# Optimization experiments

Measured on AMD Instinct MI355X. Metric: run time of the kernel, lower is better.

The kernel has to match this reference:

```python
import jax, jax.numpy as jnp
import numpy as np

K = 20

def lrelu(x):
    return jnp.where(x >= 0, x, 0.2 * x)

def get_graph_feature(x, k):
    # x: (B, N, C) channel-last. Returns (B, N, k, 2C) = [neighbor - x, x].
    inner = jnp.einsum('bnc,bmc->bnm', x, x)          # (B, N, N)
    sq = jnp.sum(x * x, axis=-1)                       # (B, N)
    # negative squared distance; top-k gives nearest neighbors (incl. self)
    neg_dist = 2.0 * inner - sq[:, :, None] - sq[:, None, :]
    _, idx = jax.lax.top_k(neg_dist, k)                # (B, N, k)
    neigh = jnp.take_along_axis(x[:, None, :, :], idx[:, :, :, None], axis=2)  # (B, N, k, C)
    center = jnp.broadcast_to(x[:, :, None, :], neigh.shape)
    return jnp.concatenate([neigh - center, center], axis=-1)

def setup_inputs() -> dict:
    key = jax.random.key(0)
    ks = jax.random.split(key, 12)
    B, N, input_dim = 32, 2048, 6
    emb_dim, out_dim = 1024, 40
    def w(k_, shape):
        fan_in = shape[-1]
        return jax.random.normal(k_, shape, dtype=jnp.float32) * (1.0 / np.sqrt(fan_in))
    return {
        'x':  jax.random.normal(ks[0], (B, N, input_dim), dtype=jnp.float32),
        'W1': w(ks[1], (64, 6)),            # conv1: 1x1 conv, no bias
        'W2': w(ks[2], (64, 128)),          # conv2
        'W5': w(ks[3], (emb_dim, 128)),     # conv5 (1d)
        'W3': w(ks[4], (32, input_dim - 3)),# conv3
        'W4': w(ks[5], (64, 32)),           # conv4
        'L1': w(ks[6], (128, (emb_dim + 64) * 2)),  # linear1, no bias
        'L2w': w(ks[7], (64, 128)),
        'L2b': jnp.zeros((64,), dtype=jnp.float32),
        'L3w': w(ks[8], (out_dim, 64)),
        'L3b': jnp.zeros((out_dim,), dtype=jnp.float32),
    }

def reference(x, W1, W2, W5, W3, W4, L1, L2w, L2b, L3w, L3b):
    x_pos = x[:, :, :3]       # (B, N, 3)
    x_feat = x[:, :, 3:]      # (B, N, input_dim-3)

    # EdgeConv block 1
    e = get_graph_feature(x_pos, K)                       # (B, N, k, 6)
    e = lrelu(jnp.einsum('bnkc,oc->bnko', e, W1))         # (B, N, k, 64)
    x1 = jnp.max(e, axis=2)                               # (B, N, 64)

    # EdgeConv block 2
    e = get_graph_feature(x1, K)                          # (B, N, k, 128)
    e = lrelu(jnp.einsum('bnkc,oc->bnko', e, W2))         # (B, N, k, 64)
    x2 = jnp.max(e, axis=2)                               # (B, N, 64)

    # conv5 over concatenated features
    h = jnp.concatenate([x1, x2], axis=-1)                # (B, N, 128)
    h = lrelu(jnp.einsum('bnc,oc->bno', h, W5))           # (B, N, emb)
    g = jnp.concatenate([jnp.max(h, axis=1), jnp.mean(h, axis=1)], axis=-1)  # (B, 2*emb)

    # per-point feature MLP (conv3 -> conv4)
    f = lrelu(jnp.einsum('bnc,oc->bno', x_feat, W3))      # (B, N, 32)
    f = lrelu(jnp.einsum('bnc,oc->bno', f, W4))           # (B, N, 64)
    fg = jnp.concatenate([jnp.max(f, axis=1), jnp.mean(f, axis=1)], axis=-1)  # (B, 128)

    z = jnp.concatenate([g, fg], axis=-1)                 # (B, (emb+64)*2)
    z = lrelu(z @ L1.T)
    z = lrelu(z @ L2w.T + L2b)
    return z @ L3w.T + L3b                                # (B, output)
```

## Files before the change

### kernel.cpp

```cpp
#include <hip/hip_runtime.h>
#include <math.h>

#define B_ 32
#define N_ 2048
#define KNN 20
#define FINF 3.402823466e38f
#define SCAP 192

typedef __attribute__((ext_vector_type(8))) short short8;
typedef __attribute__((ext_vector_type(4))) float f32x4;

#define OFF_X1   ((size_t)0)
#define OFF_X2   (OFF_X1 + (size_t)B_*N_*64*4)
#define OFF_SQ1  (OFF_X2 + (size_t)B_*N_*64*4)
#define OFF_IDX1 (OFF_SQ1 + (size_t)B_*N_*4)
#define OFF_IDX2 (OFF_IDX1 + (size_t)B_*N_*KNN*4)
#define OFF_PMAX (OFF_IDX2 + (size_t)B_*N_*KNN*4)
#define OFF_PSUM (OFF_PMAX + (size_t)B_*16*1024*4)
#define OFF_G    (OFF_PSUM + (size_t)B_*16*1024*4)
#define OFF_FG   (OFF_G + (size_t)B_*2048*4)
#define OFF_DIST (OFF_FG + (size_t)B_*128*4)
#define OFF_P    OFF_DIST
#define OFF_Q    (OFF_P   + (size_t)B_*N_*64*4)
#define OFF_XHI  (OFF_Q   + (size_t)B_*N_*64*4)
#define OFF_XLO  (OFF_XHI + (size_t)B_*N_*128*2)
#define OFF_WHI  OFF_IDX1
#define OFF_WLO  (OFF_WHI + (size_t)1024*128*2)

__device__ __forceinline__ float lrelu(float x) { return x >= 0.0f ? x : 0.2f * x; }

__device__ __forceinline__ void bf16split(float a, unsigned short& hi, unsigned short& lo) {
    unsigned u = __float_as_uint(a);
    unsigned r16 = (u + 0x7fffu + ((u >> 16) & 1u)) >> 16;
    hi = (unsigned short)r16;
    float l = a - __uint_as_float(r16 << 16);
    unsigned ul = __float_as_uint(l);
    lo = (unsigned short)((ul + 0x7fffu + ((ul >> 16) & 1u)) >> 16);
}

template<class F>
__device__ __forceinline__ void wave_top20_slow(const float (&v)[32], int lane, int* out20, F idxf) {
    unsigned alive = 0xffffffffu;
    for (int sel = 0; sel < 20; ++sel) {
        float bv = -FINF;
        int bm = 0x7fffffff;
#pragma unroll
        for (int j = 0; j < 32; ++j) {
            bool a = (alive >> j) & 1u;
            bool better = a && (v[j] > bv);
            bv = better ? v[j] : bv;
            bm = better ? idxf(j) : bm;
        }
#pragma unroll
        for (int off = 32; off; off >>= 1) {
            float ov = __shfl_xor(bv, off, 64);
            int   om = __shfl_xor(bm, off, 64);
            bool take = (ov > bv) || (ov == bv && om < bm);
            bv = take ? ov : bv;
            bm = take ? om : bm;
        }
        if (lane == 0) out20[sel] = bm;
#pragma unroll
        for (int j = 0; j < 32; ++j)
            if (idxf(j) == bm) alive &= ~(1u << j);
    }
}

template<class F>
__device__ __forceinline__ void wave_top20_fast(const float (&v)[32], int lane,
                                                float* sval, int* sidx, int* out20, F idxf) {
    float lm = v[0];
#pragma unroll
    for (int j = 1; j < 32; ++j) lm = fmaxf(lm, v[j]);
    float s = lm;
#pragma unroll
    for (int k = 2; k <= 64; k <<= 1) {
#pragma unroll
        for (int j2 = k >> 1; j2 > 0; j2 >>= 1) {
            float o = __shfl_xor(s, j2, 64);
            bool up = ((lane & k) == 0);
            bool high = ((lane & j2) != 0);
            s = (high == up) ? fmaxf(s, o) : fminf(s, o);
        }
    }
    float that = __shfl(s, 44, 64);
    int cnt = 0;
    unsigned long long below = (lane == 63) ? 0xffffffffffffffffull >> 1
                                            : ((1ull << lane) - 1ull);
#pragma unroll
    for (int j = 0; j < 32; ++j) {
        bool p = (v[j] >= that);
        unsigned long long mk = __ballot(p);
        if (p) {
            int slot = cnt + (int)__popcll(mk & below);
            if (slot < SCAP) { sval[slot] = v[j]; sidx[slot] = idxf(j); }
        }
        cnt += (int)__popcll(mk);
    }
    int S = cnt;
    if (S > SCAP) {
        wave_top20_slow(v, lane, out20, idxf);
        return;
    }
    if (S <= 64) {
        bool ok = lane < S;
        float cv = ok ? sval[lane] : -FINF;
        int   cm = ok ? sidx[lane] : 0x7fffffff;
#pragma unroll
        for (int k = 2; k <= 64; k <<= 1) {
#pragma unroll
            for (int j2 = k >> 1; j2 > 0; j2 >>= 1) {
                float ov = __shfl_xor(cv, j2, 64);
                int   om = __shfl_xor(cm, j2, 64);
                bool up = ((lane & k) == 0);
                bool high = ((lane & j2) != 0);
                bool cur_first = (cv > ov) || (cv == ov && cm < om);
                bool take = (high == up) ? cur_first : !cur_first;
                cv = take ? ov : cv;
                cm = take ? om : cm;
            }
        }
        if (lane < 20) out20[lane] = cm;
    } else {
        float cv[3]; int cm[3]; unsigned alive = 0;
#pragma unroll
        for (int r = 0; r < 3; ++r) {
            int i = r * 64 + lane;
            bool ok = i < S;
            float vv = sval[i];
            int   mm = sidx[i];
            cv[r] = ok ? vv : -FINF;
            cm[r] = ok ? mm : 0x7fffffff;
            if (ok) alive |= 1u << r;
        }
        for (int sel = 0; sel < 20; ++sel) {
            float bv = -FINF; int bm = 0x7fffffff;
#pragma unroll
            for (int r = 0; r < 3; ++r) {
                bool a = (alive >> r) & 1u;
                bool better = a && (cv[r] > bv || (cv[r] == bv && cm[r] < bm));
                bv = better ? cv[r] : bv;
                bm = better ? cm[r] : bm;
            }
#pragma unroll
            for (int off = 32; off; off >>= 1) {
                float ov = __shfl_xor(bv, off, 64);
                int   om = __shfl_xor(bm, off, 64);
                bool take = (ov > bv) || (ov == bv && om < bm);
                bv = take ? ov : bv;
                bm = take ? om : bm;
            }
            if (lane == 0) out20[sel] = bm;
#pragma unroll
            for (int r = 0; r < 3; ++r)
                if (cm[r] == bm) alive &= ~(1u << r);
        }
    }
}

__global__ __launch_bounds__(256) void k12_knn_conv1(const float* __restrict__ x,
                                                     const float* __restrict__ W1,
                                                     float* __restrict__ x1,
                                                     float* __restrict__ sq1) {
    __shared__ float sP[N_ * 3];
    __shared__ float sval[4][SCAP];
    __shared__ int   sidx[4][SCAP];
    __shared__ int   sOut[4][20];
    int tid = threadIdx.x;
    int wid = tid >> 6, lane = tid & 63;
    int row = blockIdx.x * 4 + wid;
    int b = row >> 11, n = row & 2047;
    const float* xb = x + (size_t)b * N_ * 6;
    for (int m = tid; m < N_; m += 256) {
        float4 f = *(const float4*)(xb + m * 6);
        sP[m*3+0] = f.x; sP[m*3+1] = f.y; sP[m*3+2] = f.z;
    }
    __syncthreads();
    float cx = sP[n*3+0], cy = sP[n*3+1], cz = sP[n*3+2];
    float sqn = cx*cx + cy*cy + cz*cz;
    float v[32];
#pragma unroll
    for (int j = 0; j < 32; ++j) {
        int m = lane + (j << 6);
        float mx_ = sP[m*3+0], my = sP[m*3+1], mz = sP[m*3+2];
        float inner = cx*mx_ + cy*my + cz*mz;
        float sqm = mx_*mx_ + my*my + mz*mz;
        v[j] = 2.0f*inner - sqn - sqm;
    }
    wave_top20_fast(v, lane, sval[wid], sidx[wid], sOut[wid],
                    [lane](int j) { return lane + (j << 6); });
    int o = lane;
    float w0 = W1[o*6+0], w1 = W1[o*6+1], w2 = W1[o*6+2];
    float w3 = W1[o*6+3], w4 = W1[o*6+4], w5 = W1[o*6+5];
    float base = w3*cx + w4*cy + w5*cz;
    float mx = -FINF;
#pragma unroll
    for (int k = 0; k < KNN; ++k) {
        int m = sOut[wid][k];
        float dx = sP[m*3+0]-cx, dy = sP[m*3+1]-cy, dz = sP[m*3+2]-cz;
        float s = base + w0*dx + w1*dy + w2*dz;
        mx = fmaxf(mx, lrelu(s));
    }
    x1[(size_t)row*64 + o] = mx;
    float sq = mx*mx;
#pragma unroll
    for (int off = 32; off; off >>= 1) sq += __shfl_xor(sq, off, 64);
    if (o == 0) sq1[row] = sq;
}

__global__ __launch_bounds__(256) void k3_dist(const float* __restrict__ x1,
                                               const float* __restrict__ sq1,
                                               float* __restrict__ dist, int b0) {
    __shared__ float sA[32][128];
    __shared__ float sB[32][128];
    int t = blockIdx.x;
    int I = (int)((sqrtf(8.0f*t + 1.0f) - 1.0f) * 0.5f);
    while ((I+1)*(I+2)/2 <= t) ++I;
    while (I*(I+1)/2 > t) --I;
    int J = t - I*(I+1)/2;
    int b = b0 + blockIdx.y;
    const float* Xb  = x1  + (size_t)b * N_ * 64;
    const float* sqb = sq1 + (size_t)b * N_;
    float* Db = dist + (size_t)blockIdx.y * N_ * N_;
    int i0 = I*128, j0 = J*128;
    int tid = threadIdx.x;
    float acc[8][8] = {};
    for (int kt = 0; kt < 64; kt += 32) {
#pragma unroll
        for (int l = 0; l < 4; ++l) {
            int v = l*256 + tid;
            int i = v >> 3, cg = (v & 7) << 2;
            float4 fa = *(const float4*)(Xb + (size_t)(i0+i)*64 + kt + cg);
            sA[cg+0][i] = fa.x; sA[cg+1][i] = fa.y; sA[cg+2][i] = fa.z; sA[cg+3][i] = fa.w;
            float4 fb = *(const float4*)(Xb + (size_t)(j0+i)*64 + kt + cg);
            sB[cg+0][i] = fb.x; sB[cg+1][i] = fb.y; sB[cg+2][i] = fb.z; sB[cg+3][i] = fb.w;
        }
        __syncthreads();
        int ti = (tid & 15) * 8, tj = (tid >> 4) * 8;
#pragma unroll 4
        for (int c = 0; c < 32; ++c) {
            float a[8], w[8];
            *(float4*)&a[0] = *(const float4*)&sA[c][ti];
            *(float4*)&a[4] = *(const float4*)&sA[c][ti+4];
            *(float4*)&w[0] = *(const float4*)&sB[c][tj];
            *(float4*)&w[4] = *(const float4*)&sB[c][tj+4];
#pragma unroll
            for (int ii = 0; ii < 8; ++ii)
#pragma unroll
                for (int jj = 0; jj < 8; ++jj)
                    acc[ii][jj] = fmaf(a[ii], w[jj], acc[ii][jj]);
        }
        __syncthreads();
    }
    int ti = (tid & 15) * 8, tj = (tid >> 4) * 8;
    float sqi[8], sqj[8];
#pragma unroll
    for (int ii = 0; ii < 8; ++ii) sqi[ii] = sqb[i0 + ti + ii];
#pragma unroll
    for (int jj = 0; jj < 8; ++jj) sqj[jj] = sqb[j0 + tj + jj];
#pragma unroll
    for (int ii = 0; ii < 8; ++ii) {
        float ov[8];
#pragma unroll
        for (int jj = 0; jj < 8; ++jj) ov[jj] = 2.0f*acc[ii][jj] - sqi[ii] - sqj[jj];
        float4* p = (float4*)(Db + (size_t)(i0+ti+ii)*N_ + j0 + tj);
        p[0] = *(float4*)&ov[0]; p[1] = *(float4*)&ov[4];
    }
    if (I != J) {
#pragma unroll
        for (int jj = 0; jj < 8; ++jj) {
            float ov[8];
#pragma unroll
            for (int ii = 0; ii < 8; ++ii) ov[ii] = 2.0f*acc[ii][jj] - sqi[ii] - sqj[jj];
            float4* p = (float4*)(Db + (size_t)(j0+tj+jj)*N_ + i0 + ti);
            p[0] = *(float4*)&ov[0]; p[1] = *(float4*)&ov[4];
        }
    }
}

__global__ __launch_bounds__(256) void k4_topk(const float* __restrict__ dist,
                                               int* __restrict__ idx2, int b0) {
    __shared__ float sval[4][SCAP];
    __shared__ int   sidx[4][SCAP];
    __shared__ int   sOut[4][20];
    int wid = threadIdx.x >> 6, lane = threadIdx.x & 63;
    int lrow = blockIdx.x * 4 + wid;
    int lb = lrow >> 11, n = lrow & 2047;
    const float4* Dr4 = (const float4*)(dist + (size_t)lb * N_ * N_ + (size_t)n * N_);
    float v[32];
#pragma unroll
    for (int j4 = 0; j4 < 8; ++j4) {
        float4 f = Dr4[(j4 << 6) + lane];
        v[j4*4+0] = f.x; v[j4*4+1] = f.y; v[j4*4+2] = f.z; v[j4*4+3] = f.w;
    }
    wave_top20_fast(v, lane, sval[wid], sidx[wid], sOut[wid],
                    [lane](int j) { return (lane << 2) + ((j >> 2) << 8) + (j & 3); });
    int row = (b0 + lb) * N_ + n;
    if (lane < 20) idx2[(size_t)row*KNN + lane] = sOut[wid][lane];
}

__global__ __launch_bounds__(256) void k5pre_pq(const float* __restrict__ x1,
                                                const float* __restrict__ W2,
                                                float* __restrict__ P,
                                                float* __restrict__ Q,
                                                const float* __restrict__ W5,
                                                unsigned short* __restrict__ Whi,
                                                unsigned short* __restrict__ Wlo) {
    if (blockIdx.x >= 512) {
        int e = (blockIdx.x - 512) * 256 + threadIdx.x;
        int r = e >> 5, c4 = (e & 31) << 2;
        float4 v = *(const float4*)(W5 + (size_t)r*128 + c4);
        float a[4] = {v.x, v.y, v.z, v.w};
        unsigned short hh[4], ll[4];
#pragma unroll
        for (int i = 0; i < 4; ++i) bf16split(a[i], hh[i], ll[i]);
        size_t doff = (size_t)r*128 + c4;
        *(uint2*)(Whi + doff) = make_uint2((unsigned)hh[0] | ((unsigned)hh[1] << 16),
                                           (unsigned)hh[2] | ((unsigned)hh[3] << 16));
        *(uint2*)(Wlo + doff) = make_uint2((unsigned)ll[0] | ((unsigned)ll[1] << 16),
                                           (unsigned)ll[2] | ((unsigned)ll[3] << 16));
        return;
    }
    int w = threadIdx.x >> 6, o = threadIdx.x & 63;
    float wd[64], wc[64];
    const float* wsrc = W2 + (size_t)o * 128;
#pragma unroll
    for (int j = 0; j < 16; ++j) {
        float4 d = *(const float4*)(wsrc + j*4);
        float4 c = *(const float4*)(wsrc + 64 + j*4);
        wd[j*4+0] = d.x; wd[j*4+1] = d.y; wd[j*4+2] = d.z; wd[j*4+3] = d.w;
        wc[j*4+0] = c.x - d.x; wc[j*4+1] = c.y - d.y; wc[j*4+2] = c.z - d.z; wc[j*4+3] = c.w - d.w;
    }
    int row0 = (blockIdx.x * 4 + w) * 32;
    for (int r = 0; r < 32; ++r) {
        const float* xr = x1 + (size_t)(row0 + r) * 64;
        float p = 0.0f, q = 0.0f;
#pragma unroll
        for (int j = 0; j < 16; ++j) {
            float4 xc = *(const float4*)(xr + j*4);
            p = fmaf(wd[j*4+0], xc.x, p); q = fmaf(wc[j*4+0], xc.x, q);
            p = fmaf(wd[j*4+1], xc.y, p); q = fmaf(wc[j*4+1], xc.y, q);
            p = fmaf(wd[j*4+2], xc.z, p); q = fmaf(wc[j*4+2], xc.z, q);
            p = fmaf(wd[j*4+3], xc.w, p); q = fmaf(wc[j*4+3], xc.w, q);
        }
        P[(size_t)(row0 + r) * 64 + o] = p;
        Q[(size_t)(row0 + r) * 64 + o] = q;
    }
}

__global__ __launch_bounds__(256) void k5b_max(const float* __restrict__ P,
                                               const float* __restrict__ Q,
                                               const int* __restrict__ idx2,
                                               const float* __restrict__ x1,
                                               float* __restrict__ x2,
                                               unsigned short* __restrict__ Xhi,
                                               unsigned short* __restrict__ Xlo) {
    int w = threadIdx.x >> 6, lane = threadIdx.x & 63;
    int row = blockIdx.x * 4 + w;
    int b = row >> 11;
    float q = Q[(size_t)row * 64 + lane];
    const int* id = idx2 + (size_t)row * KNN;
    const float* Pb = P + ((size_t)b << 11) * 64;
    int midx[KNN];
#pragma unroll
    for (int k = 0; k < KNN; ++k) midx[k] = id[k];
    float mx = -FINF;
#pragma unroll
    for (int k = 0; k < KNN; ++k) {
        float p = Pb[(size_t)midx[k] * 64 + lane];
        mx = fmaxf(mx, lrelu(p + q));
    }
    x2[(size_t)row * 64 + lane] = mx;
    float x1v = x1[(size_t)row * 64 + lane];
    unsigned short h0, l0, h1, l1;
    bf16split(x1v, h0, l0);
    bf16split(mx,  h1, l1);
    size_t base = (size_t)row * 128 + lane;
    Xhi[base] = h0;      Xlo[base] = l0;
    Xhi[base + 64] = h1; Xlo[base + 64] = l1;
}

__global__ __launch_bounds__(256) void k6a_mfma(const unsigned short* __restrict__ Xhi,
                                                const unsigned short* __restrict__ Xlo,
                                                const unsigned short* __restrict__ Whi,
                                                const unsigned short* __restrict__ Wlo,
                                                float* __restrict__ pmax,
                                                float* __restrict__ psum) {
    __shared__ unsigned short sT[4][128*32];
    __shared__ float redmx[128][2], redsm[128][2];
    int tid = threadIdx.x;
    int nt = blockIdx.x >> 3, ot = blockIdx.x & 7, b = blockIdx.y;
    int wid = tid >> 6, lane = tid & 63;
    int wn = wid & 1, wo = wid >> 1;
    int sub = lane & 15, quad = lane >> 4;
    const unsigned short* gp[4];
    gp[0] = Xhi + (size_t)(b*2048 + nt*128) * 128;
    gp[1] = Xlo + (size_t)(b*2048 + nt*128) * 128;
    gp[2] = Whi + (size_t)(ot*128) * 128;
    gp[3] = Wlo + (size_t)(ot*128) * 128;
    f32x4 acc[4][4];
#pragma unroll
    for (int i = 0; i < 4; ++i)
#pragma unroll
        for (int j = 0; j < 4; ++j) acc[i][j] = (f32x4)0.0f;
    for (int kt = 0; kt < 4; ++kt) {
        int k0 = kt * 32;
        __syncthreads();
#pragma unroll
        for (int it = 0; it < 8; ++it) {
            int task = it*256 + tid;
            int tile = task >> 9, rem = task & 511;
            int row = rem >> 2, ch = rem & 3;
            uint4 d = *(const uint4*)(gp[tile] + (size_t)row*128 + k0 + ch*8);
            *(uint4*)(&sT[tile][row*32 + ch*8]) = d;
        }
        __syncthreads();
        short8 ah[4], al[4], bh[4], bl[4];
#pragma unroll
        for (int mi = 0; mi < 4; ++mi) {
            int r = wn*64 + mi*16 + sub;
            ah[mi] = *(const short8*)(&sT[0][r*32 + quad*8]);
            al[mi] = *(const short8*)(&sT[1][r*32 + quad*8]);
        }
#pragma unroll
        for (int ni = 0; ni < 4; ++ni) {
            int r = wo*64 + ni*16 + sub;
            bh[ni] = *(const short8*)(&sT[2][r*32 + quad*8]);
            bl[ni] = *(const short8*)(&sT[3][r*32 + quad*8]);
        }
#pragma unroll
        for (int mi = 0; mi < 4; ++mi)
#pragma unroll
            for (int ni = 0; ni < 4; ++ni) {
                acc[mi][ni] = __builtin_amdgcn_mfma_f32_16x16x32_bf16(ah[mi], bh[ni], acc[mi][ni], 0, 0, 0);
                acc[mi][ni] = __builtin_amdgcn_mfma_f32_16x16x32_bf16(ah[mi], bl[ni], acc[mi][ni], 0, 0, 0);
                acc[mi][ni] = __builtin_amdgcn_mfma_f32_16x16x32_bf16(al[mi], bh[ni], acc[mi][ni], 0, 0, 0);
            }
    }
#pragma unroll
    for (int ni = 0; ni < 4; ++ni) {
        float mx = -FINF, sm = 0.0f;
#pragma unroll
        for (int mi = 0; mi < 4; ++mi)
#pragma unroll
            for (int r = 0; r < 4; ++r) {
                float v = lrelu(acc[mi][ni][r]);
                mx = fmaxf(mx, v); sm += v;
            }
        mx = fmaxf(mx, __shfl_xor(mx, 16, 64));
        mx = fmaxf(mx, __shfl_xor(mx, 32, 64));
        sm += __shfl_xor(sm, 16, 64);
        sm += __shfl_xor(sm, 32, 64);
        if (quad == 0) {
            redmx[wo*64 + ni*16 + sub][wn] = mx;
            redsm[wo*64 + ni*16 + sub][wn] = sm;
        }
    }
    __syncthreads();
    if (tid < 128) {
        float mx = fmaxf(redmx[tid][0], redmx[tid][1]);
        float sm = redsm[tid][0] + redsm[tid][1];
        size_t po = ((size_t)b*16 + nt)*1024 + ot*128 + tid;
        pmax[po] = mx; psum[po] = sm;
    }
}

__global__ __launch_bounds__(256) void k6b7_fused(const float* __restrict__ pmax,
                                                  const float* __restrict__ psum,
                                                  float* __restrict__ g,
                                                  const float* __restrict__ x,
                                                  const float* __restrict__ W3,
                                                  const float* __restrict__ W4,
                                                  float* __restrict__ fg) {
    __shared__ float rmx[16*256];
    __shared__ float rsm[16*256];
    int tid = threadIdx.x;
    if (blockIdx.x < 128) {
        int t = blockIdx.x * 256 + tid;
        int b = t >> 10, o = t & 1023;
        float mx = -FINF, sm = 0.0f;
        for (int i = 0; i < 16; ++i) {
            mx = fmaxf(mx, pmax[((size_t)b*16 + i)*1024 + o]);
            sm += psum[((size_t)b*16 + i)*1024 + o];
        }
        g[(size_t)b*2048 + o] = mx;
        g[(size_t)b*2048 + 1024 + o] = sm * (1.0f/2048.0f);
        return;
    }
    int idx = blockIdx.x - 128;
    int og = idx & 3, b = idx >> 2;
    int o0 = og * 16;
    float mx[16], sm[16];
#pragma unroll
    for (int i = 0; i < 16; ++i) { mx[i] = -FINF; sm[i] = 0.0f; }
    for (int n = tid; n < N_; n += 256) {
        const float* xr = x + ((size_t)b*N_ + n)*6 + 3;
        float f0 = xr[0], f1 = xr[1], f2 = xr[2];
        float h1[32];
#pragma unroll
        for (int j = 0; j < 32; ++j) {
            float s = W3[j*3]*f0 + W3[j*3+1]*f1 + W3[j*3+2]*f2;
            h1[j] = lrelu(s);
        }
#pragma unroll
        for (int oi = 0; oi < 16; ++oi) {
            float s = 0.0f;
#pragma unroll
            for (int j = 0; j < 32; ++j) s = fmaf(W4[(o0+oi)*32 + j], h1[j], s);
            s = lrelu(s);
            mx[oi] = fmaxf(mx[oi], s); sm[oi] += s;
        }
    }
#pragma unroll
    for (int oi = 0; oi < 16; ++oi) { rmx[oi*256 + tid] = mx[oi]; rsm[oi*256 + tid] = sm[oi]; }
    __syncthreads();
    for (int s = 128; s > 0; s >>= 1) {
        if (tid < s) {
#pragma unroll
            for (int oi = 0; oi < 16; ++oi) {
                rmx[oi*256 + tid] = fmaxf(rmx[oi*256 + tid], rmx[oi*256 + tid + s]);
                rsm[oi*256 + tid] += rsm[oi*256 + tid + s];
            }
        }
        __syncthreads();
    }
    if (tid < 16) {
        fg[(size_t)b*128 + o0 + tid]      = rmx[tid*256];
        fg[(size_t)b*128 + 64 + o0 + tid] = rsm[tid*256] * (1.0f/2048.0f);
    }
}

__global__ __launch_bounds__(128) void k8_head(const float* __restrict__ g,
                                               const float* __restrict__ fg,
                                               const float* __restrict__ L1w,
                                               const float* __restrict__ L2w,
                                               const float* __restrict__ L2b,
                                               const float* __restrict__ L3w,
                                               const float* __restrict__ L3b,
                                               float* __restrict__ out) {
    __shared__ float sz[2176];
    __shared__ float s1[128];
    __shared__ float s2[64];
    int b = blockIdx.x, tid = threadIdx.x;
    for (int c = tid; c < 2048; c += 128) sz[c] = g[(size_t)b*2048 + c];
    if (tid < 128) sz[2048 + tid] = fg[(size_t)b*128 + tid];
    __syncthreads();
    {
        float a = 0.0f;
        const float* w = L1w + (size_t)tid * 2176;
        for (int c = 0; c < 2176; ++c) a = fmaf(w[c], sz[c], a);
        s1[tid] = lrelu(a);
    }
    __syncthreads();
    if (tid < 64) {
        float a = L2b[tid];
        for (int c = 0; c < 128; ++c) a = fmaf(L2w[tid*128 + c], s1[c], a);
        s2[tid] = lrelu(a);
    }
    __syncthreads();
    if (tid < 40) {
        float a = L3b[tid];
        for (int c = 0; c < 64; ++c) a = fmaf(L3w[tid*64 + c], s2[c], a);
        out[(size_t)b*40 + tid] = a;
    }
}

extern "C" void kernel_launch(void* const* d_in, const int* in_sizes, int n_in,
                              void* d_out, int out_size, void* d_ws, size_t ws_size,
                              hipStream_t stream) {
    const float* x   = (const float*)d_in[0];
    const float* W1  = (const float*)d_in[1];
    const float* W2  = (const float*)d_in[2];
    const float* W5  = (const float*)d_in[3];
    const float* W3  = (const float*)d_in[4];
    const float* W4  = (const float*)d_in[5];
    const float* L1w = (const float*)d_in[6];
    const float* L2w = (const float*)d_in[7];
    const float* L2b = (const float*)d_in[8];
    const float* L3w = (const float*)d_in[9];
    const float* L3b = (const float*)d_in[10];
    float* out = (float*)d_out;

    char* ws = (char*)d_ws;
    float* x1   = (float*)(ws + OFF_X1);
    float* x2   = (float*)(ws + OFF_X2);
    float* sq1  = (float*)(ws + OFF_SQ1);
    int*   idx2 = (int*)  (ws + OFF_IDX2);
    float* pmax = (float*)(ws + OFF_PMAX);
    float* psum = (float*)(ws + OFF_PSUM);
    float* g    = (float*)(ws + OFF_G);
    float* fg   = (float*)(ws + OFF_FG);
    float* dist = (float*)(ws + OFF_DIST);
    float* P    = (float*)(ws + OFF_P);
    float* Q    = (float*)(ws + OFF_Q);
    unsigned short* Xhi = (unsigned short*)(ws + OFF_XHI);
    unsigned short* Xlo = (unsigned short*)(ws + OFF_XLO);
    unsigned short* Whi = (unsigned short*)(ws + OFF_WHI);
    unsigned short* Wlo = (unsigned short*)(ws + OFF_WLO);

    size_t distBytes = (size_t)N_ * N_ * 4;
    size_t availB = (ws_size > OFF_DIST) ? (ws_size - OFF_DIST) : 0;
    int maxcb = (int)(availB / distBytes);
    int cb = 4;
    while (cb * 2 <= maxcb && cb * 2 <= 32) cb <<= 1;

    k12_knn_conv1<<<16384, 256, 0, stream>>>(x, W1, x1, sq1);
    for (int b0 = 0; b0 < 32; b0 += cb) {
        k3_dist<<<dim3(136, cb), 256, 0, stream>>>(x1, sq1, dist, b0);
        k4_topk<<<cb * 512, 256, 0, stream>>>(dist, idx2, b0);
    }
    k5pre_pq<<<640, 256, 0, stream>>>(x1, W2, P, Q, W5, Whi, Wlo);
    k5b_max<<<16384, 256, 0, stream>>>(P, Q, idx2, x1, x2, Xhi, Xlo);
    k6a_mfma<<<dim3(128, 32), 256, 0, stream>>>(Xhi, Xlo, Whi, Wlo, pmax, psum);
    k6b7_fused<<<256, 256, 0, stream>>>(pmax, psum, g, x, W3, W4, fg);
    k8_head<<<32, 128, 0, stream>>>(g, fg, L1w, L2w, L2b, L3w, L3b, out);
}
```

Measured before the change: 802.2 us.

## Software-pipeline distance and top-k chunks with double-buffered fused kernel

Splits the distance GEMM and top-k into device bodies and adds a fused kernel whose blocks compute the next chunk's distance matrix while other blocks run top-k on the previous chunk, using two ping-pong distance buffers. The goal is to overlap the compute-bound distance pass with the memory-bound top-k pass and cut the number of serialized launches. The trade-off is a smaller chunk size (at most 16 batches, with two buffers sharing the workspace), shared-memory use sized to the larger of the two bodies, and contention between the mixed block types.

Measured after the change: 861.8 us. 1.07x slower.

```diff
diff --git a/kernel.cpp b/kernel.cpp
--- a/kernel.cpp
+++ b/kernel.cpp
@@ -208,22 +208,21 @@
     if (o == 0) sq1[row] = sq;
 }
 
-__global__ __launch_bounds__(256) void k3_dist(const float* __restrict__ x1,
-                                               const float* __restrict__ sq1,
-                                               float* __restrict__ dist, int b0) {
-    __shared__ float sA[32][128];
-    __shared__ float sB[32][128];
-    int t = blockIdx.x;
+__device__ __forceinline__ void k3_body(const float* __restrict__ x1,
+                                        const float* __restrict__ sq1,
+                                        float* __restrict__ dist, int b0,
+                                        int t, int by, char* smem, int tid) {
+    float (*sA)[128] = (float(*)[128])smem;
+    float (*sB)[128] = (float(*)[128])(smem + 16384);
     int I = (int)((sqrtf(8.0f*t + 1.0f) - 1.0f) * 0.5f);
     while ((I+1)*(I+2)/2 <= t) ++I;
     while (I*(I+1)/2 > t) --I;
     int J = t - I*(I+1)/2;
-    int b = b0 + blockIdx.y;
+    int b = b0 + by;
     const float* Xb  = x1  + (size_t)b * N_ * 64;
     const float* sqb = sq1 + (size_t)b * N_;
-    float* Db = dist + (size_t)blockIdx.y * N_ * N_;
+    float* Db = dist + (size_t)by * N_ * N_;
     int i0 = I*128, j0 = J*128;
-    int tid = threadIdx.x;
     float acc[8][8] = {};
     for (int kt = 0; kt < 64; kt += 32) {
 #pragma unroll
@@ -278,13 +277,14 @@
     }
 }
 
-__global__ __launch_bounds__(256) void k4_topk(const float* __restrict__ dist,
-                                               int* __restrict__ idx2, int b0) {
-    __shared__ float sval[4][SCAP];
-    __shared__ int   sidx[4][SCAP];
-    __shared__ int   sOut[4][20];
-    int wid = threadIdx.x >> 6, lane = threadIdx.x & 63;
-    int lrow = blockIdx.x * 4 + wid;
+__device__ __forceinline__ void k4_body(const float* __restrict__ dist,
+                                        int* __restrict__ idx2, int b0,
+                                        int blk, char* smem, int tid) {
+    float* sval = (float*)smem;
+    int*   sidx = (int*)(smem + 4*SCAP*4);
+    int*   sOut = (int*)(smem + 8*SCAP*4);
+    int wid = tid >> 6, lane = tid & 63;
+    int lrow = blk * 4 + wid;
     int lb = lrow >> 11, n = lrow & 2047;
     const float4* Dr4 = (const float4*)(dist + (size_t)lb * N_ * N_ + (size_t)n * N_);
     float v[32];
@@ -293,10 +293,38 @@
         float4 f = Dr4[(j4 << 6) + lane];
         v[j4*4+0] = f.x; v[j4*4+1] = f.y; v[j4*4+2] = f.z; v[j4*4+3] = f.w;
     }
-    wave_top20_fast(v, lane, sval[wid], sidx[wid], sOut[wid],
+    wave_top20_fast(v, lane, sval + wid*SCAP, sidx + wid*SCAP, sOut + wid*20,
                     [lane](int j) { return (lane << 2) + ((j >> 2) << 8) + (j & 3); });
     int row = (b0 + lb) * N_ + n;
-    if (lane < 20) idx2[(size_t)row*KNN + lane] = sOut[wid][lane];
+    if (lane < 20) idx2[(size_t)row*KNN + lane] = (sOut + wid*20)[lane];
+}
+
+__global__ __launch_bounds__(256) void k3_dist(const float* __restrict__ x1,
+                                               const float* __restrict__ sq1,
+                                               float* __restrict__ dist, int b0) {
+    __shared__ char smem[32768];
+    k3_body(x1, sq1, dist, b0, blockIdx.x, blockIdx.y, smem, threadIdx.x);
+}
+
+__global__ __launch_bounds__(256) void k4_topk(const float* __restrict__ dist,
+                                               int* __restrict__ idx2, int b0) {
+    __shared__ char smem[8*SCAP*4 + 4*20*4];
+    k4_body(dist, idx2, b0, blockIdx.x, smem, threadIdx.x);
+}
+
+__global__ __launch_bounds__(256) void k34_fused(const float* __restrict__ x1,
+                                                 const float* __restrict__ sq1,
+                                                 const float* __restrict__ distRead,
+                                                 float* __restrict__ distWrite,
+                                                 int* __restrict__ idx2,
+                                                 int b0read, int b0write, int nk3) {
+    __shared__ char smem[32768];
+    if ((int)blockIdx.x < nk3) {
+        k3_body(x1, sq1, distWrite, b0write, blockIdx.x % 136, blockIdx.x / 136,
+                smem, threadIdx.x);
+    } else {
+        k4_body(distRead, idx2, b0read, blockIdx.x - nk3, smem, threadIdx.x);
+    }
 }
 
 __global__ __launch_bounds__(256) void k5pre_pq(const float* __restrict__ x1,
@@ -600,15 +628,24 @@
 
     size_t distBytes = (size_t)N_ * N_ * 4;
     size_t availB = (ws_size > OFF_DIST) ? (ws_size - OFF_DIST) : 0;
-    int maxcb = (int)(availB / distBytes);
-    int cb = 4;
-    while (cb * 2 <= maxcb && cb * 2 <= 32) cb <<= 1;
+    int cb = 1;
+    while (cb * 2 <= 16 && (size_t)(cb * 2) * 2 * distBytes <= availB) cb <<= 1;
+    int nch = 32 / cb;
+    float* dA = dist;
+    float* dB = dist + (size_t)cb * N_ * N_;
 
     k12_knn_conv1<<<16384, 256, 0, stream>>>(x, W1, x1, sq1);
-    for (int b0 = 0; b0 < 32; b0 += cb) {
-        k3_dist<<<dim3(136, cb), 256, 0, stream>>>(x1, sq1, dist, b0);
-        k4_topk<<<cb * 512, 256, 0, stream>>>(dist, idx2, b0);
-    }
+    k3_dist<<<dim3(136, cb), 256, 0, stream>>>(x1, sq1, dA, 0);
+    for (int c = 0; c + 1 < nch; ++c) {
+        float* cur = (c & 1) ? dB : dA;
+        float* nxt = (c & 1) ? dA : dB;
+        int nk3 = 136 * cb, nk4 = 512 * cb;
+        k34_fused<<<nk3 + nk4, 256, 0, stream>>>(x1, sq1, cur, nxt, idx2,
+                                                 c * cb, (c + 1) * cb, nk3);
+    }
+    float* last = ((nch - 1) & 1) ? dB : dA;
+    k4_topk<<<512 * cb, 256, 0, stream>>>(last, idx2, (nch - 1) * cb);
+
     k5pre_pq<<<640, 256, 0, stream>>>(x1, W2, P, Q, W5, Whi, Wlo);
     k5b_max<<<16384, 256, 0, stream>>>(P, Q, idx2, x1, x2, Xhi, Xlo);
     k6a_mfma<<<dim3(128, 32), 256, 0, stream>>>(Xhi, Xlo, Whi, Wlo, pmax, psum);
```
